# Kernel optimization log

Hardware: AMD Instinct MI355X
Metric: run time of the kernel (lower is better)

The kernel has to match this reference:

```python
import jax, jax.numpy as jnp
import numpy as np


def conv1x1(x, w, b):
    # x: [B, C, H, W], w: [O, C], b: [O] -> [B, O, H, W]
    return jnp.einsum('bchw,oc->bohw', x, w) + b[None, :, None, None]


def setup_inputs() -> dict:
    key = jax.random.key(0)
    ks = jax.random.split(key, 9)
    B, C, H, W = 2, 64, 96, 96
    inter = C // 2
    s = 0.05
    return {
        'x': jax.random.normal(ks[0], (B, C, H, W), dtype=jnp.float32),
        'g_w': jax.random.normal(ks[1], (inter, C), dtype=jnp.float32) * s,
        'g_b': jax.random.normal(ks[2], (inter,), dtype=jnp.float32) * s,
        'theta_w': jax.random.normal(ks[3], (inter, C), dtype=jnp.float32) * s,
        'theta_b': jax.random.normal(ks[4], (inter,), dtype=jnp.float32) * s,
        'phi_w': jax.random.normal(ks[5], (inter, C), dtype=jnp.float32) * s,
        'phi_b': jax.random.normal(ks[6], (inter,), dtype=jnp.float32) * s,
        'W_w': jax.random.normal(ks[7], (C, inter), dtype=jnp.float32) * s,
        'W_b': jax.random.normal(ks[8], (C,), dtype=jnp.float32) * s,
    }


def reference(x, g_w, g_b, theta_w, theta_b, phi_w, phi_b, W_w, W_b):
    B, C, H, W = x.shape
    inter = g_w.shape[0]
    N = H * W
    g_x = conv1x1(x, g_w, g_b).reshape(B, inter, N)          # [B, inter, N]
    theta_x = conv1x1(x, theta_w, theta_b).reshape(B, inter, N)  # [B, inter, N]
    phi_x = conv1x1(x, phi_w, phi_b).reshape(B, inter, N)    # [B, inter, N]
    # f[b, n, m] = sum_i phi[b, i, n] * theta[b, i, m]  -> [B, N, N]
    f = jnp.einsum('bin,bim->bnm', phi_x, theta_x)
    f_div_C = jax.nn.softmax(f, axis=-1)
    # y[b, n, i] = sum_m f_div_C[b, n, m] * g_x[b, i, m]
    y = jnp.einsum('bnm,bim->bni', f_div_C, g_x)             # [B, N, inter]
    y = jnp.transpose(y, (0, 2, 1)).reshape(B, inter, H, W)
    W_y = conv1x1(y, W_w, W_b)
    return W_y + x
```

## Files before the change

### kernel.cpp

```cpp
#include <hip/hip_runtime.h>
#include <cstdint>

#define BN 9216
#define NB 2
#define CIN 64
#define DI 32
#define MC 8
#define NCHUNK 288
#define LOG2E 1.4426950408889634f

typedef __attribute__((ext_vector_type(4))) float f32x4;
typedef __attribute__((ext_vector_type(8))) __bf16 bf16x8;
typedef __attribute__((ext_vector_type(4))) unsigned int u32x4;

__device__ __forceinline__ unsigned short f2bf(float f) {
    unsigned int u = __builtin_bit_cast(unsigned int, f);
    u += 0x7FFFu + ((u >> 16) & 1u);
    return (unsigned short)(u >> 16);
}
__device__ __forceinline__ unsigned int packbf(float lo, float hi) {
    return (unsigned int)f2bf(lo) | ((unsigned int)f2bf(hi) << 16);
}

__device__ __forceinline__ float exp2_hw(float x) {
    float r;
    asm("v_exp_f32 %0, %1" : "=v"(r) : "v"(x));
    return r;
}

__global__ __launch_bounds__(64) void qkv_kernel(
    const float* __restrict__ x,
    const float* __restrict__ g_w, const float* __restrict__ g_b,
    const float* __restrict__ th_w, const float* __restrict__ th_b,
    const float* __restrict__ ph_w, const float* __restrict__ ph_b,
    unsigned short* __restrict__ qT, unsigned short* __restrict__ kT,
    unsigned short* __restrict__ vv)
{
    __shared__ float wsh[3 * 8 * CIN];
    __shared__ float bsh[3 * 8];
    const int og = blockIdx.y;
    const int b = blockIdx.z;
    const int tid = threadIdx.x;
    for (int i = tid; i < 8 * CIN; i += 64) {
        const int o = i / CIN, c = i % CIN;
        wsh[0 * 512 + i] = ph_w[(size_t)(og * 8 + o) * CIN + c] * LOG2E;
        wsh[1 * 512 + i] = th_w[(size_t)(og * 8 + o) * CIN + c];
        wsh[2 * 512 + i] = g_w [(size_t)(og * 8 + o) * CIN + c];
    }
    if (tid < 8) {
        bsh[tid]      = ph_b[og * 8 + tid] * LOG2E;
        bsh[8 + tid]  = th_b[og * 8 + tid];
        bsh[16 + tid] = g_b [og * 8 + tid];
    }
    __syncthreads();

    const int n = blockIdx.x * 64 + tid;
    const float* xp = x + (size_t)b * CIN * BN + n;

    float aq[8], ak[8], av[8];
#pragma unroll
    for (int o = 0; o < 8; ++o) {
        aq[o] = bsh[o]; ak[o] = bsh[8 + o]; av[o] = bsh[16 + o];
    }
    for (int c0 = 0; c0 < CIN; c0 += 16) {
        float xv[16];
#pragma unroll
        for (int u = 0; u < 16; ++u) xv[u] = xp[(size_t)(c0 + u) * BN];
#pragma unroll
        for (int u = 0; u < 16; ++u) {
#pragma unroll
            for (int o = 0; o < 8; ++o) {
                aq[o] += wsh[0 * 512 + o * CIN + c0 + u] * xv[u];
                ak[o] += wsh[1 * 512 + o * CIN + c0 + u] * xv[u];
                av[o] += wsh[2 * 512 + o * CIN + c0 + u] * xv[u];
            }
        }
    }

    {
        unsigned short* qp = qT + ((size_t)b * BN + n) * DI + og * 8;
        u32x4 tq = {packbf(aq[0], aq[1]), packbf(aq[2], aq[3]),
                    packbf(aq[4], aq[5]), packbf(aq[6], aq[7])};
        *(u32x4*)qp = tq;
        unsigned short* kp = kT + ((size_t)b * BN + n) * DI + og * 8;
        u32x4 tk = {packbf(ak[0], ak[1]), packbf(ak[2], ak[3]),
                    packbf(ak[4], ak[5]), packbf(ak[6], ak[7])};
        *(u32x4*)kp = tk;
    }
    {
        unsigned short* vp = vv + (size_t)b * DI * BN + n;
#pragma unroll
        for (int o = 0; o < 8; ++o) vp[(size_t)(og * 8 + o) * BN] = f2bf(av[o]);
    }
}

__global__ __launch_bounds__(256) void attn_partial(
    const unsigned short* __restrict__ qT, const unsigned short* __restrict__ kT,
    const unsigned short* __restrict__ vv,
    float* __restrict__ pacc, float* __restrict__ pl)
{
    __shared__ float red_l[4][2][16];
    __shared__ float red_acc[4][2][512];

    const int b  = blockIdx.z;
    const int mc = blockIdx.y;
    const int nc = blockIdx.x;
    const int n0 = nc * 32;
    const int tid = threadIdx.x;
    const int w = tid >> 6;
    const int lane = tid & 63;
    const int h = lane >> 4;
    const int q = lane & 15;
    const int sig = 8 * (q >> 2) + (q & 3);

    const unsigned short* qTb = qT + (size_t)b * BN * DI;
    const unsigned short* kTb = kT + (size_t)b * BN * DI;
    const unsigned short* vb  = vv + (size_t)b * DI * BN;

    bf16x8 qfA = *(const bf16x8*)(qTb + ((size_t)(n0 + q)) * DI + 8 * h);
    bf16x8 qfB = *(const bf16x8*)(qTb + ((size_t)(n0 + 16 + q)) * DI + 8 * h);
    const f32x4 zero = {0.f, 0.f, 0.f, 0.f};
    f32x4 a0A = zero, a1A = zero, a0B = zero, a1B = zero;
    float lA = 0.f, lB = 0.f;

    const unsigned short* krow = kTb + (size_t)sig * DI + 8 * h;
    const unsigned short* vrow0 = vb + (size_t)q * BN + 8 * h;
    const unsigned short* vrow1 = vb + (size_t)(16 + q) * BN + 8 * h;

    int m0 = mc * 1152 + w * 32;

#define LD_K0(m) (*(const bf16x8*)(krow + (size_t)(m) * DI))
#define LD_K1(m) (*(const bf16x8*)(krow + (size_t)((m) + 4) * DI))
#define LD_V0(m) (*(const bf16x8*)(vrow0 + (m)))
#define LD_V1(m) (*(const bf16x8*)(vrow1 + (m)))

    bf16x8 ck0 = LD_K0(m0), ck1 = LD_K1(m0), cv0 = LD_V0(m0), cv1 = LD_V1(m0);

    auto compute = [&](bf16x8 k0, bf16x8 k1, bf16x8 v0, bf16x8 v1) {
        f32x4 s0A = __builtin_amdgcn_mfma_f32_16x16x32_bf16(k0, qfA, zero, 0, 0, 0);
        f32x4 s1A = __builtin_amdgcn_mfma_f32_16x16x32_bf16(k1, qfA, zero, 0, 0, 0);
        f32x4 s0B = __builtin_amdgcn_mfma_f32_16x16x32_bf16(k0, qfB, zero, 0, 0, 0);
        f32x4 s1B = __builtin_amdgcn_mfma_f32_16x16x32_bf16(k1, qfB, zero, 0, 0, 0);
        {
            float p0 = exp2_hw(s0A[0]), p1 = exp2_hw(s0A[1]);
            float p2 = exp2_hw(s0A[2]), p3 = exp2_hw(s0A[3]);
            float p4 = exp2_hw(s1A[0]), p5 = exp2_hw(s1A[1]);
            float p6 = exp2_hw(s1A[2]), p7 = exp2_hw(s1A[3]);
            lA += ((p0 + p1) + (p2 + p3)) + ((p4 + p5) + (p6 + p7));
            bf16x8 pf = {(__bf16)p0, (__bf16)p1, (__bf16)p2, (__bf16)p3,
                         (__bf16)p4, (__bf16)p5, (__bf16)p6, (__bf16)p7};
            a0A = __builtin_amdgcn_mfma_f32_16x16x32_bf16(v0, pf, a0A, 0, 0, 0);
            a1A = __builtin_amdgcn_mfma_f32_16x16x32_bf16(v1, pf, a1A, 0, 0, 0);
        }
        {
            float p0 = exp2_hw(s0B[0]), p1 = exp2_hw(s0B[1]);
            float p2 = exp2_hw(s0B[2]), p3 = exp2_hw(s0B[3]);
            float p4 = exp2_hw(s1B[0]), p5 = exp2_hw(s1B[1]);
            float p6 = exp2_hw(s1B[2]), p7 = exp2_hw(s1B[3]);
            lB += ((p0 + p1) + (p2 + p3)) + ((p4 + p5) + (p6 + p7));
            bf16x8 pf = {(__bf16)p0, (__bf16)p1, (__bf16)p2, (__bf16)p3,
                         (__bf16)p4, (__bf16)p5, (__bf16)p6, (__bf16)p7};
            a0B = __builtin_amdgcn_mfma_f32_16x16x32_bf16(v0, pf, a0B, 0, 0, 0);
            a1B = __builtin_amdgcn_mfma_f32_16x16x32_bf16(v1, pf, a1B, 0, 0, 0);
        }
    };

#pragma unroll 1
    for (int it = 0; it < 8; ++it) {
        const int mn = m0 + 128;
        bf16x8 nk0 = LD_K0(mn), nk1 = LD_K1(mn);
        bf16x8 nv0 = LD_V0(mn), nv1 = LD_V1(mn);
        compute(ck0, ck1, cv0, cv1);
        ck0 = nk0; ck1 = nk1; cv0 = nv0; cv1 = nv1;
        m0 = mn;
    }
    compute(ck0, ck1, cv0, cv1);

#undef LD_K0
#undef LD_K1
#undef LD_V0
#undef LD_V1

    lA += __shfl_xor(lA, 16, 64); lA += __shfl_xor(lA, 32, 64);
    lB += __shfl_xor(lB, 16, 64); lB += __shfl_xor(lB, 32, 64);

    if (lane < 16) { red_l[w][0][lane] = lA; red_l[w][1][lane] = lB; }

#pragma unroll
    for (int t = 0; t < 4; ++t) {
        red_acc[w][0][(4 * h + t) * 16 + q]      = a0A[t];
        red_acc[w][0][(16 + 4 * h + t) * 16 + q] = a1A[t];
        red_acc[w][1][(4 * h + t) * 16 + q]      = a0B[t];
        red_acc[w][1][(16 + 4 * h + t) * 16 + q] = a1B[t];
    }
    __syncthreads();

    {
        const int np = tid & 31;
        const int ig = tid >> 5;
        const int tt = np >> 4, qq = np & 15;
        const size_t pbase = (((size_t)b * MC + mc) * NCHUNK + nc) * 1024;
#pragma unroll
        for (int ii = 0; ii < 4; ++ii) {
            const int i = ig * 4 + ii;
            float ysum = red_acc[0][tt][i * 16 + qq] + red_acc[1][tt][i * 16 + qq]
                       + red_acc[2][tt][i * 16 + qq] + red_acc[3][tt][i * 16 + qq];
            pacc[pbase + (size_t)i * 32 + np] = ysum;
        }
        if (tid < 32) {
            float L = red_l[0][tt][qq] + red_l[1][tt][qq]
                    + red_l[2][tt][qq] + red_l[3][tt][qq];
            pl[(((size_t)b * MC + mc) * NCHUNK + nc) * 32 + np] = L;
        }
    }
}

__global__ __launch_bounds__(256) void combine_outconv(
    const float* __restrict__ pacc, const float* __restrict__ pl,
    const float* __restrict__ Ww, const float* __restrict__ Wb,
    const float* __restrict__ x, float* __restrict__ out)
{
    __shared__ float sl[MC * 32];
    __shared__ float ysh[32 * 33];
    __shared__ float WwT[32 * 65];
    __shared__ float swb[64];

    const int b  = blockIdx.y;
    const int nc = blockIdx.x;
    const int tid = threadIdx.x;
    const int n  = tid & 31;
    const int ig = tid >> 5;

    {
        sl[tid] = pl[(((size_t)b * MC + (tid >> 5)) * NCHUNK + nc) * 32 + (tid & 31)];
#pragma unroll
        for (int e = tid; e < 2048; e += 256)
            WwT[(e & 31) * 65 + (e >> 5)] = Ww[e];
        if (tid < 64) swb[tid] = Wb[tid];
    }

    float xr[8];
    const float* xp = x + ((size_t)b * CIN + ig * 8) * BN + nc * 32 + n;
#pragma unroll
    for (int oo = 0; oo < 8; ++oo) xr[oo] = xp[(size_t)oo * BN];

    __syncthreads();

    {
        float L = 0.f;
#pragma unroll
        for (int mc2 = 0; mc2 < MC; ++mc2) L += sl[mc2 * 32 + n];
        const float inv = 1.0f / L;

        const size_t pb0 = (((size_t)b * MC) * NCHUNK + nc) * 1024;
#pragma unroll
        for (int ii = 0; ii < 4; ++ii) {
            const int i = ig * 4 + ii;
            float y = 0.f;
#pragma unroll
            for (int mc2 = 0; mc2 < MC; ++mc2)
                y += pacc[pb0 + (size_t)mc2 * NCHUNK * 1024 + (size_t)i * 32 + n];
            ysh[i * 33 + n] = y * inv;
        }
    }
    __syncthreads();

    {
        float acc[8];
#pragma unroll
        for (int oo = 0; oo < 8; ++oo) acc[oo] = swb[ig * 8 + oo];
#pragma unroll
        for (int i = 0; i < 32; ++i) {
            float yv = ysh[i * 33 + n];
#pragma unroll
            for (int oo = 0; oo < 8; ++oo)
                acc[oo] += WwT[i * 65 + ig * 8 + oo] * yv;
        }
        float* op = out + ((size_t)b * CIN + ig * 8) * BN + nc * 32 + n;
#pragma unroll
        for (int oo = 0; oo < 8; ++oo) op[(size_t)oo * BN] = acc[oo] + xr[oo];
    }
}

extern "C" void kernel_launch(void* const* d_in, const int* in_sizes, int n_in,
                              void* d_out, int out_size, void* d_ws, size_t ws_size,
                              hipStream_t stream)
{
    const float* x    = (const float*)d_in[0];
    const float* g_w  = (const float*)d_in[1];
    const float* g_b  = (const float*)d_in[2];
    const float* th_w = (const float*)d_in[3];
    const float* th_b = (const float*)d_in[4];
    const float* ph_w = (const float*)d_in[5];
    const float* ph_b = (const float*)d_in[6];
    const float* W_w  = (const float*)d_in[7];
    const float* W_b  = (const float*)d_in[8];
    float* out = (float*)d_out;

    char* ws = (char*)d_ws;
    unsigned short* qT = (unsigned short*)(ws);
    unsigned short* kT = (unsigned short*)(ws + 1179648);
    unsigned short* vv = (unsigned short*)(ws + 2359296);
    float* pacc = (float*)(ws + 3538944);
    float* pl   = (float*)(ws + 22413312);

    dim3 g1(BN / 64, 4, NB);
    qkv_kernel<<<g1, 64, 0, stream>>>(x, g_w, g_b, th_w, th_b, ph_w, ph_b,
                                      qT, kT, vv);
    dim3 g2(NCHUNK, MC, NB);
    attn_partial<<<g2, 256, 0, stream>>>(qT, kT, vv, pacc, pl);
    dim3 g3(NCHUNK, NB);
    combine_outconv<<<g3, 256, 0, stream>>>(pacc, pl, W_w, W_b, x, out);
}
```

Measured before the change: 154.2 us.

## Halve key splits, rebalance QKV and combine kernels' work decomposition

The attention split count along the key dimension drops from 8 to 4, so each attention block loops over twice as many keys and writes half as many partial accumulators, which cuts partial-sum traffic and combine reads. The QKV projection kernel now uses 256-thread blocks with 4 output channels per block instead of 64 threads with 8. The combine/output-conv kernel is split into half-chunks of 16 positions to keep the block count up. The cost is fewer attention blocks, so there is less parallelism and possibly worse occupancy balance across CUs.

```diff
diff --git a/kernel.cpp b/kernel.cpp
--- a/kernel.cpp
+++ b/kernel.cpp
@@ -5,13 +5,13 @@
 #define NB 2
 #define CIN 64
 #define DI 32
-#define MC 8
+#define MC 4
 #define NCHUNK 288
 #define LOG2E 1.4426950408889634f
 
 typedef __attribute__((ext_vector_type(4))) float f32x4;
 typedef __attribute__((ext_vector_type(8))) __bf16 bf16x8;
-typedef __attribute__((ext_vector_type(4))) unsigned int u32x4;
+typedef __attribute__((ext_vector_type(2))) unsigned int u32x2;
 
 __device__ __forceinline__ unsigned short f2bf(float f) {
     unsigned int u = __builtin_bit_cast(unsigned int, f);
@@ -28,7 +28,7 @@
     return r;
 }
 
-__global__ __launch_bounds__(64) void qkv_kernel(
+__global__ __launch_bounds__(256) void qkv_kernel(
     const float* __restrict__ x,
     const float* __restrict__ g_w, const float* __restrict__ g_b,
     const float* __restrict__ th_w, const float* __restrict__ th_b,
@@ -36,31 +36,31 @@
     unsigned short* __restrict__ qT, unsigned short* __restrict__ kT,
     unsigned short* __restrict__ vv)
 {
-    __shared__ float wsh[3 * 8 * CIN];
-    __shared__ float bsh[3 * 8];
+    __shared__ float wsh[3 * 4 * CIN];
+    __shared__ float bsh[12];
     const int og = blockIdx.y;
     const int b = blockIdx.z;
     const int tid = threadIdx.x;
-    for (int i = tid; i < 8 * CIN; i += 64) {
-        const int o = i / CIN, c = i % CIN;
-        wsh[0 * 512 + i] = ph_w[(size_t)(og * 8 + o) * CIN + c] * LOG2E;
-        wsh[1 * 512 + i] = th_w[(size_t)(og * 8 + o) * CIN + c];
-        wsh[2 * 512 + i] = g_w [(size_t)(og * 8 + o) * CIN + c];
-    }
-    if (tid < 8) {
-        bsh[tid]      = ph_b[og * 8 + tid] * LOG2E;
-        bsh[8 + tid]  = th_b[og * 8 + tid];
-        bsh[16 + tid] = g_b [og * 8 + tid];
+    if (tid < 4 * CIN) {
+        const int o = tid / CIN, c = tid % CIN;
+        wsh[0 * 256 + tid] = ph_w[(size_t)(og * 4 + o) * CIN + c] * LOG2E;
+        wsh[1 * 256 + tid] = th_w[(size_t)(og * 4 + o) * CIN + c];
+        wsh[2 * 256 + tid] = g_w [(size_t)(og * 4 + o) * CIN + c];
+    }
+    if (tid < 4) {
+        bsh[tid]     = ph_b[og * 4 + tid] * LOG2E;
+        bsh[4 + tid] = th_b[og * 4 + tid];
+        bsh[8 + tid] = g_b [og * 4 + tid];
     }
     __syncthreads();
 
-    const int n = blockIdx.x * 64 + tid;
+    const int n = blockIdx.x * 256 + tid;
     const float* xp = x + (size_t)b * CIN * BN + n;
 
-    float aq[8], ak[8], av[8];
-#pragma unroll
-    for (int o = 0; o < 8; ++o) {
-        aq[o] = bsh[o]; ak[o] = bsh[8 + o]; av[o] = bsh[16 + o];
+    float aq[4], ak[4], av[4];
+#pragma unroll
+    for (int o = 0; o < 4; ++o) {
+        aq[o] = bsh[o]; ak[o] = bsh[4 + o]; av[o] = bsh[8 + o];
     }
     for (int c0 = 0; c0 < CIN; c0 += 16) {
         float xv[16];
@@ -69,28 +69,26 @@
 #pragma unroll
         for (int u = 0; u < 16; ++u) {
 #pragma unroll
-            for (int o = 0; o < 8; ++o) {
-                aq[o] += wsh[0 * 512 + o * CIN + c0 + u] * xv[u];
-                ak[o] += wsh[1 * 512 + o * CIN + c0 + u] * xv[u];
-                av[o] += wsh[2 * 512 + o * CIN + c0 + u] * xv[u];
+            for (int o = 0; o < 4; ++o) {
+                aq[o] += wsh[0 * 256 + o * CIN + c0 + u] * xv[u];
+                ak[o] += wsh[1 * 256 + o * CIN + c0 + u] * xv[u];
+                av[o] += wsh[2 * 256 + o * CIN + c0 + u] * xv[u];
             }
         }
     }
 
     {
-        unsigned short* qp = qT + ((size_t)b * BN + n) * DI + og * 8;
-        u32x4 tq = {packbf(aq[0], aq[1]), packbf(aq[2], aq[3]),
-                    packbf(aq[4], aq[5]), packbf(aq[6], aq[7])};
-        *(u32x4*)qp = tq;
-        unsigned short* kp = kT + ((size_t)b * BN + n) * DI + og * 8;
-        u32x4 tk = {packbf(ak[0], ak[1]), packbf(ak[2], ak[3]),
-                    packbf(ak[4], ak[5]), packbf(ak[6], ak[7])};
-        *(u32x4*)kp = tk;
+        unsigned short* qp = qT + ((size_t)b * BN + n) * DI + og * 4;
+        u32x2 tq = {packbf(aq[0], aq[1]), packbf(aq[2], aq[3])};
+        *(u32x2*)qp = tq;
+        unsigned short* kp = kT + ((size_t)b * BN + n) * DI + og * 4;
+        u32x2 tk = {packbf(ak[0], ak[1]), packbf(ak[2], ak[3])};
+        *(u32x2*)kp = tk;
     }
     {
         unsigned short* vp = vv + (size_t)b * DI * BN + n;
 #pragma unroll
-        for (int o = 0; o < 8; ++o) vp[(size_t)(og * 8 + o) * BN] = f2bf(av[o]);
+        for (int o = 0; o < 4; ++o) vp[(size_t)(og * 4 + o) * BN] = f2bf(av[o]);
     }
 }
 
@@ -127,7 +125,7 @@
     const unsigned short* vrow0 = vb + (size_t)q * BN + 8 * h;
     const unsigned short* vrow1 = vb + (size_t)(16 + q) * BN + 8 * h;
 
-    int m0 = mc * 1152 + w * 32;
+    int m0 = mc * 2304 + w * 32;
 
 #define LD_K0(m) (*(const bf16x8*)(krow + (size_t)(m) * DI))
 #define LD_K1(m) (*(const bf16x8*)(krow + (size_t)((m) + 4) * DI))
@@ -166,7 +164,7 @@
     };
 
 #pragma unroll 1
-    for (int it = 0; it < 8; ++it) {
+    for (int it = 0; it < 17; ++it) {
         const int mn = m0 + 128;
         bf16x8 nk0 = LD_K0(mn), nk1 = LD_K1(mn);
         bf16x8 nv0 = LD_V0(mn), nv1 = LD_V1(mn);
@@ -220,65 +218,72 @@
     const float* __restrict__ Ww, const float* __restrict__ Wb,
     const float* __restrict__ x, float* __restrict__ out)
 {
-    __shared__ float sl[MC * 32];
-    __shared__ float ysh[32 * 33];
+    __shared__ float sl[MC * 16];
+    __shared__ float ysh[32 * 17];
     __shared__ float WwT[32 * 65];
     __shared__ float swb[64];
 
-    const int b  = blockIdx.y;
-    const int nc = blockIdx.x;
-    const int tid = threadIdx.x;
-    const int n  = tid & 31;
-    const int ig = tid >> 5;
-
-    {
-        sl[tid] = pl[(((size_t)b * MC + (tid >> 5)) * NCHUNK + nc) * 32 + (tid & 31)];
+    const int b    = blockIdx.y;
+    const int nc2  = blockIdx.x;
+    const int nc   = nc2 >> 1;
+    const int half = nc2 & 1;
+    const int tid  = threadIdx.x;
+    const int n16  = tid & 15;
+    const int grp  = tid >> 4;
+    const int np   = half * 16 + n16;
+
+    {
+        if (tid < MC * 16) {
+            const int mc = tid >> 4, j = tid & 15;
+            sl[tid] = pl[(((size_t)b * MC + mc) * NCHUNK + nc) * 32
+                         + half * 16 + j];
+        }
 #pragma unroll
         for (int e = tid; e < 2048; e += 256)
             WwT[(e & 31) * 65 + (e >> 5)] = Ww[e];
         if (tid < 64) swb[tid] = Wb[tid];
     }
 
-    float xr[8];
-    const float* xp = x + ((size_t)b * CIN + ig * 8) * BN + nc * 32 + n;
-#pragma unroll
-    for (int oo = 0; oo < 8; ++oo) xr[oo] = xp[(size_t)oo * BN];
+    float xr[4];
+    const float* xp = x + ((size_t)b * CIN + grp * 4) * BN + nc2 * 16 + n16;
+#pragma unroll
+    for (int oo = 0; oo < 4; ++oo) xr[oo] = xp[(size_t)oo * BN];
 
     __syncthreads();
 
     {
         float L = 0.f;
 #pragma unroll
-        for (int mc2 = 0; mc2 < MC; ++mc2) L += sl[mc2 * 32 + n];
+        for (int mc2 = 0; mc2 < MC; ++mc2) L += sl[mc2 * 16 + n16];
         const float inv = 1.0f / L;
 
         const size_t pb0 = (((size_t)b * MC) * NCHUNK + nc) * 1024;
 #pragma unroll
-        for (int ii = 0; ii < 4; ++ii) {
-            const int i = ig * 4 + ii;
+        for (int ii = 0; ii < 2; ++ii) {
+            const int i = grp * 2 + ii;
             float y = 0.f;
 #pragma unroll
             for (int mc2 = 0; mc2 < MC; ++mc2)
-                y += pacc[pb0 + (size_t)mc2 * NCHUNK * 1024 + (size_t)i * 32 + n];
-            ysh[i * 33 + n] = y * inv;
+                y += pacc[pb0 + (size_t)mc2 * NCHUNK * 1024 + (size_t)i * 32 + np];
+            ysh[i * 17 + n16] = y * inv;
         }
     }
     __syncthreads();
 
     {
-        float acc[8];
-#pragma unroll
-        for (int oo = 0; oo < 8; ++oo) acc[oo] = swb[ig * 8 + oo];
+        float acc[4];
+#pragma unroll
+        for (int oo = 0; oo < 4; ++oo) acc[oo] = swb[grp * 4 + oo];
 #pragma unroll
         for (int i = 0; i < 32; ++i) {
-            float yv = ysh[i * 33 + n];
-#pragma unroll
-            for (int oo = 0; oo < 8; ++oo)
-                acc[oo] += WwT[i * 65 + ig * 8 + oo] * yv;
-        }
-        float* op = out + ((size_t)b * CIN + ig * 8) * BN + nc * 32 + n;
-#pragma unroll
-        for (int oo = 0; oo < 8; ++oo) op[(size_t)oo * BN] = acc[oo] + xr[oo];
+            float yv = ysh[i * 17 + n16];
+#pragma unroll
+            for (int oo = 0; oo < 4; ++oo)
+                acc[oo] += WwT[i * 65 + grp * 4 + oo] * yv;
+        }
+        float* op = out + ((size_t)b * CIN + grp * 4) * BN + nc2 * 16 + n16;
+#pragma unroll
+        for (int oo = 0; oo < 4; ++oo) op[(size_t)oo * BN] = acc[oo] + xr[oo];
     }
 }
 
@@ -302,13 +307,13 @@
     unsigned short* kT = (unsigned short*)(ws + 1179648);
     unsigned short* vv = (unsigned short*)(ws + 2359296);
     float* pacc = (float*)(ws + 3538944);
-    float* pl   = (float*)(ws + 22413312);
-
-    dim3 g1(BN / 64, 4, NB);
-    qkv_kernel<<<g1, 64, 0, stream>>>(x, g_w, g_b, th_w, th_b, ph_w, ph_b,
-                                      qT, kT, vv);
+    float* pl   = (float*)(ws + 12976128);
+
+    dim3 g1(BN / 256, 8, NB);
+    qkv_kernel<<<g1, 256, 0, stream>>>(x, g_w, g_b, th_w, th_b, ph_w, ph_b,
+                                       qT, kT, vv);
     dim3 g2(NCHUNK, MC, NB);
     attn_partial<<<g2, 256, 0, stream>>>(qT, kT, vv, pacc, pl);
-    dim3 g3(NCHUNK, NB);
+    dim3 g3(NCHUNK * 2, NB);
     combine_outconv<<<g3, 256, 0, stream>>>(pacc, pl, W_w, W_b, x, out);
 }
```

New measurement: 156.3 us. No clear change (+1.4%).
